# Kernel tuning notes

Hardware: AMD Instinct MI355X
Metric: run time of the kernel (lower is better)

The kernel has to match this reference:

```python
import jax, jax.numpy as jnp
import numpy as np

DIM = 512
HEADS = 16
HEAD_DIM = DIM // HEADS
SCALE = HEAD_DIM ** -0.5


def setup_inputs() -> dict:
    key = jax.random.key(0)
    k = jax.random.split(key, 6)
    B_, N = 2048, 49
    nW = 64
    x = jax.random.normal(k[0], (B_, N, DIM), dtype=jnp.float32)
    mask = jax.random.normal(k[1], (nW, N, N), dtype=jnp.float32)
    W_qkv = jax.random.normal(k[2], (3 * DIM, DIM), dtype=jnp.float32) * 0.02
    b_qkv = jnp.zeros((3 * DIM,), dtype=jnp.float32)
    W_proj = jax.random.normal(k[3], (DIM, DIM), dtype=jnp.float32) * 0.02
    b_proj = jnp.zeros((DIM,), dtype=jnp.float32)
    return {"x": x, "mask": mask, "W_qkv": W_qkv, "b_qkv": b_qkv,
            "W_proj": W_proj, "b_proj": b_proj}


def reference(x, mask, W_qkv, b_qkv, W_proj, b_proj):
    B_, N, C = x.shape
    H, d = HEADS, HEAD_DIM
    nW = mask.shape[0]
    # qkv projection: [B_, N, 3, H, d] -> q,k,v each [B_, H, N, d]
    qkv = (x @ W_qkv.T + b_qkv).reshape(B_, N, 3, H, d)
    qkv = jnp.transpose(qkv, (2, 0, 3, 1, 4))
    q, k, v = qkv[0], qkv[1], qkv[2]
    attn = jnp.einsum('bhnd,bhmd->bhnm', q * SCALE, k)  # [B_, H, N, N]
    # add per-window additive mask, broadcast over B_//nW groups and heads
    attn = attn.reshape(B_ // nW, nW, H, N, N) + mask[None, :, None, :, :]
    attn = attn.reshape(B_, H, N, N)
    attn = jax.nn.softmax(attn, axis=-1)
    out = jnp.einsum('bhnm,bhmd->bhnd', attn, v)  # [B_, H, N, d]
    out = jnp.transpose(out, (0, 2, 1, 3)).reshape(B_, N, C)
    return out @ W_proj.T + b_proj
```

## Files before the change

kernel.cpp:

```cpp
#include <hip/hip_runtime.h>


typedef unsigned short ushort_t;
typedef __bf16 bf16x8 __attribute__((ext_vector_type(8)));
typedef float f32x4 __attribute__((ext_vector_type(4)));
typedef unsigned short us8 __attribute__((ext_vector_type(8)));

#define SCALE_F 0.17677669529663687f
constexpr size_t QKV_REG = 2048ULL * 16 * 49 * 32;

__device__ __forceinline__ ushort_t f2bf(float f) {
  unsigned u = __builtin_bit_cast(unsigned, f);
  u += 0x7FFFu + ((u >> 16) & 1u);
  return (ushort_t)(u >> 16);
}

__device__ __forceinline__ void gload_lds16(const void* g, void* l) {
  __builtin_amdgcn_global_load_lds(
      (const __attribute__((address_space(1))) void*)g,
      (__attribute__((address_space(3))) void*)l, 16, 0, 0);
}

__global__ __launch_bounds__(256) void k_cvt(const float* __restrict__ in,
                                             ushort_t* __restrict__ out, int n4) {
  int i = blockIdx.x * blockDim.x + threadIdx.x;
  if (i >= n4) return;
  float4 v = reinterpret_cast<const float4*>(in)[i];
  ushort4 o = make_ushort4(f2bf(v.x), f2bf(v.y), f2bf(v.z), f2bf(v.w));
  reinterpret_cast<ushort4*>(out)[i] = o;
}

template <int EPI>
__global__ __launch_bounds__(256) void k_gemm(const ushort_t* __restrict__ A,
                                              const ushort_t* __restrict__ W,
                                              const float* __restrict__ bias,
                                              ushort_t* __restrict__ out_qkv,
                                              float* __restrict__ out_f,
                                              int nt_o) {
  __shared__ __align__(16) ushort_t As[128][64];
  __shared__ __align__(16) ushort_t Ws[128][64];

  const int tid  = threadIdx.x;
  const int lane = tid & 63;
  const int wv   = tid >> 6;
  const int wr   = wv >> 1, wc = wv & 1;
  const int bm   = blockIdx.x / nt_o;
  const int bo   = blockIdx.x - bm * nt_o;
  const size_t m0 = (size_t)bm * 128;
  const int o0    = bo * 128;

  f32x4 acc[4][4];
#pragma unroll
  for (int i = 0; i < 4; i++)
#pragma unroll
    for (int j = 0; j < 4; j++) acc[i][j] = f32x4{0.f, 0.f, 0.f, 0.f};

  const int srow   = wv * 32 + (lane >> 3);
  const int schunk = (lane & 7) * 8;

  for (int kt = 0; kt < 8; ++kt) {
    const int k0 = kt * 64;
#pragma unroll
    for (int i = 0; i < 4; i++) {
      const ushort_t* g = A + (m0 + srow + i * 8) * 512 + k0 + schunk;
      gload_lds16(g, &As[wv * 32 + i * 8][0]);
    }
#pragma unroll
    for (int i = 0; i < 4; i++) {
      const ushort_t* g = W + (size_t)(o0 + srow + i * 8) * 512 + k0 + schunk;
      gload_lds16(g, &Ws[wv * 32 + i * 8][0]);
    }
    __syncthreads();
#pragma unroll
    for (int kk = 0; kk < 2; ++kk) {
      const int kc = kk * 32 + (lane >> 4) * 8;
      uint4 ar[4], br[4];
#pragma unroll
      for (int mi = 0; mi < 4; mi++)
        ar[mi] = *reinterpret_cast<const uint4*>(&As[wr * 64 + mi * 16 + (lane & 15)][kc]);
#pragma unroll
      for (int ni = 0; ni < 4; ni++)
        br[ni] = *reinterpret_cast<const uint4*>(&Ws[wc * 64 + ni * 16 + (lane & 15)][kc]);
#pragma unroll
      for (int mi = 0; mi < 4; mi++)
#pragma unroll
        for (int ni = 0; ni < 4; ni++)
          acc[mi][ni] = __builtin_amdgcn_mfma_f32_16x16x32_bf16(
              __builtin_bit_cast(bf16x8, ar[mi]),
              __builtin_bit_cast(bf16x8, br[ni]), acc[mi][ni], 0, 0, 0);
    }
    __syncthreads();
  }

  const int colbase = lane & 15;
  const int rowgrp  = (lane >> 4) * 4;

  if constexpr (EPI == 1) {
#pragma unroll
    for (int ni = 0; ni < 4; ni++) {
      const int o = o0 + wc * 64 + ni * 16 + colbase;
      const float bv = bias[o];
#pragma unroll
      for (int mi = 0; mi < 4; mi++) {
        const size_t mrow = m0 + wr * 64 + mi * 16 + rowgrp;
#pragma unroll
        for (int r = 0; r < 4; r++)
          out_f[(mrow + r) * 512 + o] = acc[mi][ni][r] + bv;
      }
    }
  } else {
#pragma unroll
    for (int mi = 0; mi < 4; mi++) {
#pragma unroll
      for (int r = 0; r < 4; r++) {
        const int t = (int)m0 + wr * 64 + mi * 16 + rowgrp + r;
        const int b = t / 49;
        const int n = t - b * 49;
#pragma unroll
        for (int ni = 0; ni < 4; ni++) {
          const int o = o0 + wc * 64 + ni * 16 + colbase;
          const int which = o >> 9;
          const int h = (o >> 5) & 15;
          const int dd = o & 31;
          const size_t dst = (size_t)which * QKV_REG +
                             (((size_t)b * 16 + h) * 49 + n) * 32 + dd;
          out_qkv[dst] = f2bf(acc[mi][ni][r] + bias[o]);
        }
      }
    }
  }
}

__global__ __launch_bounds__(256) void k_attn(const ushort_t* __restrict__ qkv,
                                              const float* __restrict__ mask,
                                              ushort_t* __restrict__ aout) {
  __shared__ __align__(16) ushort_t Vt[32][64];
  __shared__ __align__(16) ushort_t Ps[4][16][64];

  const int tid  = threadIdx.x;
  const int lane = tid & 63;
  const int mt   = tid >> 6;
  const int bh   = blockIdx.x;
  const int b    = bh >> 4, h = bh & 15;
  const int w    = b & 63;
  const size_t base = (size_t)bh * (49 * 32);
  const ushort_t* qb = qkv + base;
  const ushort_t* kb = qkv + QKV_REG + base;
  const ushort_t* vb = qkv + 2 * QKV_REG + base;

  reinterpret_cast<uint4*>(&Vt[0][0])[tid] = make_uint4(0, 0, 0, 0);
  __syncthreads();
  if (tid < 196) {
    const int n = tid >> 2, d0 = (tid & 3) * 8;
    uint4 raw = *reinterpret_cast<const uint4*>(vb + n * 32 + d0);
    us8 e = __builtin_bit_cast(us8, raw);
#pragma unroll
    for (int j = 0; j < 8; j++) Vt[d0 + j][n] = e[j];
  }
  __syncthreads();

  const int arow = lane & 15;
  const int kc   = (lane >> 4) * 8;

  uint4 qraw = *reinterpret_cast<const uint4*>(qb + (mt * 16 + arow) * 32 + kc);
  bf16x8 qa = __builtin_bit_cast(bf16x8, qraw);
  f32x4 s[4];
#pragma unroll
  for (int ni = 0; ni < 4; ni++) {
    uint4 kraw = *reinterpret_cast<const uint4*>(kb + (ni * 16 + arow) * 32 + kc);
    f32x4 z = {0.f, 0.f, 0.f, 0.f};
    s[ni] = __builtin_amdgcn_mfma_f32_16x16x32_bf16(
        qa, __builtin_bit_cast(bf16x8, kraw), z, 0, 0, 0);
  }

  const int rg = (lane >> 4) * 4;
  float rsum[4];
#pragma unroll
  for (int r = 0; r < 4; r++) {
    const int qr = mt * 16 + rg + r;
    float sv[4];
    float mx = -1e30f;
#pragma unroll
    for (int ni = 0; ni < 4; ni++) {
      const int col = ni * 16 + arow;
      float v;
      if (qr < 49 && col < 49)
        v = s[ni][r] * SCALE_F + mask[(size_t)w * 2401 + qr * 49 + col];
      else
        v = -1e30f;
      sv[ni] = v;
      mx = fmaxf(mx, v);
    }
#pragma unroll
    for (int off = 1; off < 16; off <<= 1) mx = fmaxf(mx, __shfl_xor(mx, off));
    float sum = 0.f;
#pragma unroll
    for (int ni = 0; ni < 4; ni++) {
      float p = __expf(sv[ni] - mx);
      sum += p;
      Ps[mt][rg + r][ni * 16 + arow] = f2bf(p);
    }
#pragma unroll
    for (int off = 1; off < 16; off <<= 1) sum += __shfl_xor(sum, off);
    rsum[r] = sum;
  }

  __syncthreads();

  f32x4 o0 = {0.f, 0.f, 0.f, 0.f}, o1 = {0.f, 0.f, 0.f, 0.f};
#pragma unroll
  for (int kk = 0; kk < 2; kk++) {
    uint4 praw = *reinterpret_cast<const uint4*>(&Ps[mt][arow][kk * 32 + kc]);
    bf16x8 pa = __builtin_bit_cast(bf16x8, praw);
    uint4 v0 = *reinterpret_cast<const uint4*>(&Vt[arow][kk * 32 + kc]);
    uint4 v1 = *reinterpret_cast<const uint4*>(&Vt[16 + arow][kk * 32 + kc]);
    o0 = __builtin_amdgcn_mfma_f32_16x16x32_bf16(pa, __builtin_bit_cast(bf16x8, v0), o0, 0, 0, 0);
    o1 = __builtin_amdgcn_mfma_f32_16x16x32_bf16(pa, __builtin_bit_cast(bf16x8, v1), o1, 0, 0, 0);
  }

#pragma unroll
  for (int r = 0; r < 4; r++) {
    const int qr = mt * 16 + rg + r;
    if (qr < 49) {
      const float inv = 1.f / rsum[r];
      aout[((size_t)b * 49 + qr) * 512 + h * 32 + arow]      = f2bf(o0[r] * inv);
      aout[((size_t)b * 49 + qr) * 512 + h * 32 + 16 + arow] = f2bf(o1[r] * inv);
    }
  }
}

extern "C" void kernel_launch(void* const* d_in, const int* in_sizes, int n_in,
                              void* d_out, int out_size, void* d_ws, size_t ws_size,
                              hipStream_t stream) {
  const float* x      = (const float*)d_in[0];
  const float* mask   = (const float*)d_in[1];
  const float* W_qkv  = (const float*)d_in[2];
  const float* b_qkv  = (const float*)d_in[3];
  const float* W_proj = (const float*)d_in[4];
  const float* b_proj = (const float*)d_in[5];
  float* out = (float*)d_out;

  ushort_t* ws     = (ushort_t*)d_ws;
  ushort_t* xb     = ws;
  ushort_t* qkvb   = ws + 51380224UL;
  ushort_t* aoutb  = ws + 205520896UL;
  ushort_t* wqkvb  = ws + 256901120UL;
  ushort_t* wprojb = ws + 257687552UL;

  const int n4x = 51380224 / 4, n4q = 786432 / 4, n4p = 262144 / 4;
  k_cvt<<<(n4x + 255) / 256, 256, 0, stream>>>(x, xb, n4x);
  k_cvt<<<(n4q + 255) / 256, 256, 0, stream>>>(W_qkv, wqkvb, n4q);
  k_cvt<<<(n4p + 255) / 256, 256, 0, stream>>>(W_proj, wprojb, n4p);

  k_gemm<0><<<784 * 12, 256, 0, stream>>>(xb, wqkvb, b_qkv, qkvb, nullptr, 12);

  k_attn<<<2048 * 16, 256, 0, stream>>>(qkvb, mask, aoutb);

  k_gemm<1><<<784 * 4, 256, 0, stream>>>(aoutb, wprojb, b_proj, nullptr, out, 4);
}
```

Before: 657.5 us.

## XOR-swizzle LDS tiles in GEMM and attention, remap GEMM block order

Applies an XOR swizzle on 16-byte chunks to the GEMM A/W shared tiles, the attention P tile and the transposed V tile, so MFMA fragment reads stop hitting the same LDS banks. The GEMM also remaps block IDs across 8 groups (likely for XCD locality on MI355X) so neighbouring tiles share cache. The swizzled write and read indexing must match exactly, and the block remap assumes the grid size is divisible by 8.

Result: faster. 592.9 us (-9.8%).

```diff
diff --git a/kernel.cpp b/kernel.cpp
--- a/kernel.cpp
+++ b/kernel.cpp
@@ -44,8 +44,11 @@
   const int lane = tid & 63;
   const int wv   = tid >> 6;
   const int wr   = wv >> 1, wc = wv & 1;
-  const int bm   = blockIdx.x / nt_o;
-  const int bo   = blockIdx.x - bm * nt_o;
+
+  const int cpx = gridDim.x >> 3;
+  const int lid = (blockIdx.x & 7) * cpx + (blockIdx.x >> 3);
+  const int bm  = lid / nt_o;
+  const int bo  = lid - bm * nt_o;
   const size_t m0 = (size_t)bm * 128;
   const int o0    = bo * 128;
 
@@ -56,7 +59,7 @@
     for (int j = 0; j < 4; j++) acc[i][j] = f32x4{0.f, 0.f, 0.f, 0.f};
 
   const int srow   = wv * 32 + (lane >> 3);
-  const int schunk = (lane & 7) * 8;
+  const int schunk = (((lane & 7) ^ (lane >> 3)) * 8);
 
   for (int kt = 0; kt < 8; ++kt) {
     const int k0 = kt * 64;
@@ -71,16 +74,18 @@
       gload_lds16(g, &Ws[wv * 32 + i * 8][0]);
     }
     __syncthreads();
+    const int fr = lane & 15;
 #pragma unroll
     for (int kk = 0; kk < 2; ++kk) {
-      const int kc = kk * 32 + (lane >> 4) * 8;
+      const int ch = kk * 4 + (lane >> 4);
+      const int cb = ((ch ^ (lane & 7)) << 3);
       uint4 ar[4], br[4];
 #pragma unroll
       for (int mi = 0; mi < 4; mi++)
-        ar[mi] = *reinterpret_cast<const uint4*>(&As[wr * 64 + mi * 16 + (lane & 15)][kc]);
+        ar[mi] = *reinterpret_cast<const uint4*>(&As[wr * 64 + mi * 16 + fr][cb]);
 #pragma unroll
       for (int ni = 0; ni < 4; ni++)
-        br[ni] = *reinterpret_cast<const uint4*>(&Ws[wc * 64 + ni * 16 + (lane & 15)][kc]);
+        br[ni] = *reinterpret_cast<const uint4*>(&Ws[wc * 64 + ni * 16 + fr][cb]);
 #pragma unroll
       for (int mi = 0; mi < 4; mi++)
 #pragma unroll
@@ -155,7 +160,9 @@
     uint4 raw = *reinterpret_cast<const uint4*>(vb + n * 32 + d0);
     us8 e = __builtin_bit_cast(us8, raw);
 #pragma unroll
-    for (int j = 0; j < 8; j++) Vt[d0 + j][n] = e[j];
+    for (int j = 0; j < 8; j++) {
+      Vt[d0 + j][(((n >> 3) ^ j) << 3) | (n & 7)] = e[j];
+    }
   }
   __syncthreads();
 
@@ -194,11 +201,13 @@
 #pragma unroll
     for (int off = 1; off < 16; off <<= 1) mx = fmaxf(mx, __shfl_xor(mx, off));
     float sum = 0.f;
+    const int prow = rg + r;
 #pragma unroll
     for (int ni = 0; ni < 4; ni++) {
       float p = __expf(sv[ni] - mx);
       sum += p;
-      Ps[mt][rg + r][ni * 16 + arow] = f2bf(p);
+      const int pcol = ni * 16 + arow;
+      Ps[mt][prow][(((pcol >> 3) ^ (prow & 7)) << 3) | (pcol & 7)] = f2bf(p);
     }
 #pragma unroll
     for (int off = 1; off < 16; off <<= 1) sum += __shfl_xor(sum, off);
@@ -210,10 +219,12 @@
   f32x4 o0 = {0.f, 0.f, 0.f, 0.f}, o1 = {0.f, 0.f, 0.f, 0.f};
 #pragma unroll
   for (int kk = 0; kk < 2; kk++) {
-    uint4 praw = *reinterpret_cast<const uint4*>(&Ps[mt][arow][kk * 32 + kc]);
+    const int ch = kk * 4 + (lane >> 4);
+    const int cb = ((ch ^ (lane & 7)) << 3);
+    uint4 praw = *reinterpret_cast<const uint4*>(&Ps[mt][arow][cb]);
     bf16x8 pa = __builtin_bit_cast(bf16x8, praw);
-    uint4 v0 = *reinterpret_cast<const uint4*>(&Vt[arow][kk * 32 + kc]);
-    uint4 v1 = *reinterpret_cast<const uint4*>(&Vt[16 + arow][kk * 32 + kc]);
+    uint4 v0 = *reinterpret_cast<const uint4*>(&Vt[arow][cb]);
+    uint4 v1 = *reinterpret_cast<const uint4*>(&Vt[16 + arow][cb]);
     o0 = __builtin_amdgcn_mfma_f32_16x16x32_bf16(pa, __builtin_bit_cast(bf16x8, v0), o0, 0, 0, 0);
     o1 = __builtin_amdgcn_mfma_f32_16x16x32_bf16(pa, __builtin_bit_cast(bf16x8, v1), o1, 0, 0, 0);
   }
```
